# Optimization experiments

Hardware: AMD Instinct MI355X
Metric: run time of the kernel (lower is better)

The kernel has to match this reference:

```python
import math
import jax, jax.numpy as jnp
import numpy as np

H, C, PQ, PV = 8, 256, 8, 12   # no_heads, c_hidden, no_qk_points, no_v_points
INF, EPS = 1e5, 1e-8

def quat_to_rot(q):
    w, x, y, z = q[..., 0], q[..., 1], q[..., 2], q[..., 3]
    r = jnp.stack([
        1 - 2*(y*y + z*z), 2*(x*y - w*z),     2*(x*z + w*y),
        2*(x*y + w*z),     1 - 2*(x*x + z*z), 2*(y*z - w*x),
        2*(x*z - w*y),     2*(y*z + w*x),     1 - 2*(x*x + y*y),
    ], axis=-1)
    return r.reshape(q.shape[:-1] + (3, 3))

def setup_inputs() -> dict:
    key = jax.random.key(0)
    ks = jax.random.split(key, 16)
    B, N, CS, CZ = 1, 512, 384, 128
    s = jax.random.normal(ks[0], (B, N, CS), jnp.float32)
    z = jax.random.normal(ks[1], (B, N, N, CZ), jnp.float32) * 0.1
    quat = jax.random.normal(ks[2], (B, N, 4), jnp.float32)
    quat = quat / jnp.linalg.norm(quat, axis=-1, keepdims=True)
    rot = quat_to_rot(quat)                       # [B,N,3,3] valid rotations
    trans = jax.random.normal(ks[3], (B, N, 3), jnp.float32) * 10.0
    mask = jnp.ones((B, N), jnp.float32)
    g = lambda k, sh: jax.random.normal(k, sh, jnp.float32) * 0.02
    params = dict(
        wq=g(ks[4], (CS, H*C)), bq=jnp.zeros((H*C,), jnp.float32),
        wkv=g(ks[5], (CS, 2*H*C)), bkv=jnp.zeros((2*H*C,), jnp.float32),
        wqp=g(ks[6], (CS, H*PQ*3)), bqp=jnp.zeros((H*PQ*3,), jnp.float32),
        wkvp=g(ks[7], (CS, H*(PQ+PV)*3)), bkvp=jnp.zeros((H*(PQ+PV)*3,), jnp.float32),
        wb=g(ks[8], (CZ, H)), bb=jnp.zeros((H,), jnp.float32),
        wz=g(ks[9], (CZ, CZ//4)), bz=jnp.zeros((CZ//4,), jnp.float32),
        head_weights=jnp.full((H,), 0.541324854612918, jnp.float32),  # softplus^-1(1)
        wo=g(ks[10], (H*(C + 4*PV + CZ//4), CS)), bo=jnp.zeros((CS,), jnp.float32),
    )
    return dict(s=s, z=z, rot=rot, trans=trans, mask=mask, **params)

def reference(s, z, rot, trans, mask, wq, bq, wkv, bkv, wqp, bqp, wkvp, bkvp, wb, bb, wz, bz, head_weights, wo, bo):
    B, N, CS = s.shape
    q = (s @ wq + bq).reshape(B, N, H, C)
    kv = (s @ wkv + bkv).reshape(B, N, H, 2 * C)
    k, v = kv[..., :C], kv[..., C:]

    def split_pts(x):  # torch split-into-3 + stack(-1): [B,N,3*M] -> [B,N,M,3]
        return jnp.moveaxis(x.reshape(B, N, 3, -1), -2, -1)

    def apply_rigid(p):  # global frame: R @ p + t
        return jnp.einsum('bnij,bnpj->bnpi', rot, p) + trans[:, :, None, :]

    q_pts = apply_rigid(split_pts(s @ wqp + bqp)).reshape(B, N, H, PQ, 3)
    kv_pts = apply_rigid(split_pts(s @ wkvp + bkvp)).reshape(B, N, H, PQ + PV, 3)
    k_pts, v_pts = kv_pts[..., :PQ, :], kv_pts[..., PQ:, :]

    b_bias = z @ wb + bb                                  # [B,Ni,Nj,H]
    a = jnp.einsum('bihc,bjhc->bhij', q, k) * math.sqrt(1.0 / (3 * C))
    a = a + math.sqrt(1.0 / 3) * jnp.moveaxis(b_bias, -1, 1)

    disp = q_pts[:, :, None] - k_pts[:, None]             # [B,Ni,Nj,H,PQ,3]
    pt_att = jnp.sum(disp * disp, axis=-1)                # [B,Ni,Nj,H,PQ]
    hw = jax.nn.softplus(head_weights) * math.sqrt(1.0 / (3 * (PQ * 9.0 / 2)))
    pt_att = -0.5 * jnp.sum(pt_att * hw[None, None, None, :, None], axis=-1)  # [B,Ni,Nj,H]

    sq_mask = INF * (mask[:, :, None] * mask[:, None, :] - 1.0)
    a = a + jnp.moveaxis(pt_att, -1, 1) + sq_mask[:, None]
    a = jax.nn.softmax(a, axis=-1)                        # [B,H,Ni,Nj]

    o = jnp.einsum('bhij,bjhc->bihc', a, v).reshape(B, N, H * C)

    o_pt = jnp.einsum('bhij,bjhpd->bihpd', a, v_pts)      # [B,N,H,PV,3] global
    o_pt = jnp.einsum('bnji,bnhpj->bnhpi', rot, o_pt - trans[:, :, None, None, :])  # invert_apply
    o_pt_norm = jnp.sqrt(jnp.sum(o_pt * o_pt, axis=-1) + EPS).reshape(B, N, H * PV)
    o_pt_flat = o_pt.reshape(B, N, H * PV, 3)

    pair_z = z @ wz + bz                                  # [B,Ni,Nj,CZ//4]
    o_pair = jnp.einsum('bhij,bijd->bihd', a, pair_z).reshape(B, N, -1)

    feats = jnp.concatenate(
        [o, o_pt_flat[..., 0], o_pt_flat[..., 1], o_pt_flat[..., 2], o_pt_norm, o_pair], axis=-1)
    return feats @ wo + bo
```

## Files before the change

kernel.cpp:

```cpp
#include <hip/hip_runtime.h>


#define OFF_QBH    0
#define OFF_KBH    524288
#define OFF_VB     1048576
#define OFF_QPRAW  2097152
#define OFF_KVPRAW 2195456
#define OFF_QPTS   2441216
#define OFF_KVPTS  2539520
#define OFF_BBIAS  2785280
#define OFF_PAIRZT 3833856
#define OFF_ATTNH  8028160
#define OFF_FEATSB 9076736
#define OFF_WCAT   9764864
#define OFF_WTALL  9767936
#define OFF_VPT    11082752
#define OFF_WOT    11803648
#define OFF_QPTH   12319744
#define OFF_QPTL   12385280
#define OFF_KPTH   12450816
#define OFF_KPTL   12516352
#define OFF_QP2    12581888
#define OFF_KP2    12585984

typedef __attribute__((ext_vector_type(8))) short short8;
typedef __attribute__((ext_vector_type(4))) float f32x4;

__device__ __forceinline__ unsigned short f2bf(float f) {
  union { float f; unsigned u; } v; v.f = f;
  unsigned u = v.u;
  unsigned r = (u + 0x7fffu + ((u >> 16) & 1u)) >> 16;
  return (unsigned short)r;
}
__device__ __forceinline__ float bf2f(unsigned short h) {
  union { unsigned u; float f; } v; v.u = ((unsigned)h) << 16; return v.f;
}
__device__ __forceinline__ short8 pack8(float4 a, float4 b) {
  short8 r;
  r[0] = (short)f2bf(a.x); r[1] = (short)f2bf(a.y);
  r[2] = (short)f2bf(a.z); r[3] = (short)f2bf(a.w);
  r[4] = (short)f2bf(b.x); r[5] = (short)f2bf(b.y);
  r[6] = (short)f2bf(b.z); r[7] = (short)f2bf(b.w);
  return r;
}

__global__ __launch_bounds__(256) void prep_wT_all(
    const float* __restrict__ wq, const float* __restrict__ wkv,
    const float* __restrict__ wqp, const float* __restrict__ wkvp,
    unsigned short* __restrict__ wTall) {
  const int ntile = blockIdx.x, kt = blockIdx.y;
  const float* src; int Nsrc, nloc0;
  const int ng0 = ntile * 64;
  if (ntile < 32)      { src = wq;   Nsrc = 2048; nloc0 = ng0; }
  else if (ntile < 96) { src = wkv;  Nsrc = 4096; nloc0 = ng0 - 2048; }
  else if (ntile < 99) { src = wqp;  Nsrc = 192;  nloc0 = ng0 - 6144; }
  else                 { src = wkvp; Nsrc = 480;  nloc0 = ng0 - 6336; }
  __shared__ float tile[64][65];
  const int t = threadIdx.x;
  const int r = t >> 2, cs = (t & 3) * 16;
#pragma unroll
  for (int i = 0; i < 16; i += 4) {
    int n = nloc0 + cs + i;
    float4 v;
    if (n + 3 < Nsrc) v = *(const float4*)(src + (size_t)(kt * 64 + r) * Nsrc + n);
    else {
      v.x = (n + 0 < Nsrc) ? src[(size_t)(kt * 64 + r) * Nsrc + n + 0] : 0.f;
      v.y = (n + 1 < Nsrc) ? src[(size_t)(kt * 64 + r) * Nsrc + n + 1] : 0.f;
      v.z = (n + 2 < Nsrc) ? src[(size_t)(kt * 64 + r) * Nsrc + n + 2] : 0.f;
      v.w = (n + 3 < Nsrc) ? src[(size_t)(kt * 64 + r) * Nsrc + n + 3] : 0.f;
    }
    tile[r][cs + i + 0] = v.x; tile[r][cs + i + 1] = v.y;
    tile[r][cs + i + 2] = v.z; tile[r][cs + i + 3] = v.w;
  }
  __syncthreads();
  const int nr = t >> 2, ks = (t & 3) * 16;
  unsigned short ov[16];
#pragma unroll
  for (int i = 0; i < 16; i++) ov[i] = f2bf(tile[ks + i][nr]);
  unsigned short* dst = wTall + (size_t)(ng0 + nr) * 384 + kt * 64 + ks;
  *(uint4*)(dst) = *(const uint4*)&ov[0];
  *(uint4*)(dst + 8) = *(const uint4*)&ov[8];
}

__global__ __launch_bounds__(256) void prep_woT(
    const float* __restrict__ wo, unsigned short* __restrict__ woT) {
  const int kt = blockIdx.x, ntile = blockIdx.y;
  __shared__ float tile[64][65];
  const int t = threadIdx.x;
  const int r = t >> 2, cs = (t & 3) * 16;
#pragma unroll
  for (int i = 0; i < 16; i += 4) {
    float4 v = *(const float4*)(wo + (size_t)(kt * 64 + r) * 384 + ntile * 64 + cs + i);
    tile[r][cs + i + 0] = v.x; tile[r][cs + i + 1] = v.y;
    tile[r][cs + i + 2] = v.z; tile[r][cs + i + 3] = v.w;
  }
  __syncthreads();
  const int nr = t >> 2, ks = (t & 3) * 16;
  unsigned short ov[16];
#pragma unroll
  for (int i = 0; i < 16; i++) ov[i] = f2bf(tile[ks + i][nr]);
  unsigned short* dst = woT + (size_t)(ntile * 64 + nr) * 2688 + kt * 64 + ks;
  *(uint4*)(dst) = *(const uint4*)&ov[0];
  *(uint4*)(dst + 8) = *(const uint4*)&ov[8];
}

__global__ __launch_bounds__(256) void proj_mfma(
    const float* __restrict__ s, const unsigned short* __restrict__ wTall,
    const float* __restrict__ bq, const float* __restrict__ bkv,
    const float* __restrict__ bqp, const float* __restrict__ bkvp,
    unsigned short* __restrict__ qbh, unsigned short* __restrict__ kbh,
    float* __restrict__ vb, float* __restrict__ qpraw, float* __restrict__ kvpraw) {
  const int bx = blockIdx.x, row0 = blockIdx.y * 64;
  const int lane = threadIdx.x & 63, wv = threadIdx.x >> 6;
  const int quad = lane >> 4, m = lane & 15;
  const int n0 = bx * 64;
  const float* srow = s + (size_t)(row0 + wv * 16 + m) * 384;
  f32x4 acc[4];
#pragma unroll
  for (int nt = 0; nt < 4; nt++) acc[nt] = (f32x4){0.f, 0.f, 0.f, 0.f};

#pragma unroll
  for (int ksx = 0; ksx < 12; ksx++) {
    const int c0 = ksx * 32 + quad * 8;
    float4 a0 = *(const float4*)(srow + c0);
    float4 a1 = *(const float4*)(srow + c0 + 4);
    short8 af = pack8(a0, a1);
#pragma unroll
    for (int nt = 0; nt < 4; nt++) {
      short8 bf = *(const short8*)(wTall + (size_t)(n0 + nt * 16 + m) * 384 + c0);
      acc[nt] = __builtin_amdgcn_mfma_f32_16x16x32_bf16(af, bf, acc[nt], 0, 0, 0);
    }
  }

  const int rbase = row0 + wv * 16 + quad * 4;
#pragma unroll
  for (int nt = 0; nt < 4; nt++) {
    const int col = n0 + nt * 16 + m;
    if (n0 < 2048) {
      const float bias = bq[col];
#pragma unroll
      for (int r = 0; r < 4; r++)
        qbh[(size_t)(rbase + r) * 2048 + col] = f2bf(acc[nt][r] + bias);
    } else if (n0 < 6144) {
      const int ckv = col - 2048;
      const float bias = bkv[ckv];
      const int hh = ckv >> 9, c = ckv & 511;
      if (c < 256) {
#pragma unroll
        for (int r = 0; r < 4; r++)
          kbh[(size_t)(rbase + r) * 2048 + hh * 256 + c] = f2bf(acc[nt][r] + bias);
      } else {
#pragma unroll
        for (int r = 0; r < 4; r++)
          vb[(size_t)(rbase + r) * 2048 + hh * 256 + (c - 256)] = acc[nt][r] + bias;
      }
    } else if (n0 < 6336) {
      const int cq = col - 6144;
      const float bias = bqp[cq];
#pragma unroll
      for (int r = 0; r < 4; r++)
        qpraw[(size_t)(rbase + r) * 192 + cq] = acc[nt][r] + bias;
    } else {
      const int ck = col - 6336;
      if (ck < 480) {
        const float bias = bkvp[ck];
#pragma unroll
        for (int r = 0; r < 4; r++)
          kvpraw[(size_t)(rbase + r) * 480 + ck] = acc[nt][r] + bias;
      }
    }
  }
}

__global__ __launch_bounds__(256) void rigid_pts(
    const float* __restrict__ qpraw, const float* __restrict__ kvpraw,
    const float* __restrict__ rot, const float* __restrict__ trans,
    float* __restrict__ qpts, float* __restrict__ kvpts) {
  int gid = blockIdx.x * 256 + threadIdx.x;
  int n = gid / 224, r = gid % 224;
  const float* R  = rot + n * 9;
  const float* tr = trans + n * 3;
  float px, py, pz; float* dst;
  if (r < 64) {
    const float* src = qpraw + (size_t)n * 192;
    px = src[r]; py = src[64 + r]; pz = src[128 + r];
    dst = qpts + ((size_t)n * 64 + r) * 3;
  } else {
    int p = r - 64;
    const float* src = kvpraw + (size_t)n * 480;
    px = src[p]; py = src[160 + p]; pz = src[320 + p];
    dst = kvpts + ((size_t)n * 160 + p) * 3;
  }
  dst[0] = R[0] * px + R[1] * py + R[2] * pz + tr[0];
  dst[1] = R[3] * px + R[4] * py + R[5] * pz + tr[1];
  dst[2] = R[6] * px + R[7] * py + R[8] * pz + tr[2];
}

__global__ __launch_bounds__(256) void pts_planes(
    const float* __restrict__ qpts, const float* __restrict__ kvpts,
    unsigned short* __restrict__ qptH, unsigned short* __restrict__ qptL,
    unsigned short* __restrict__ kptH, unsigned short* __restrict__ kptL,
    float* __restrict__ qp2g, float* __restrict__ kp2g) {
  const int row = blockIdx.x * 256 + threadIdx.x;
  const int h = blockIdx.y;
  {
    const float* src = qpts + ((size_t)row * 64 + h * 8) * 3;
    unsigned short hi[32], lo[32]; float s2 = 0.f;
#pragma unroll
    for (int w = 0; w < 24; w++) {
      float x = src[w];
      hi[w] = f2bf(x); lo[w] = f2bf(x - bf2f(hi[w]));
      s2 += x * x;
    }
#pragma unroll
    for (int w = 24; w < 32; w++) { hi[w] = 0; lo[w] = 0; }
    unsigned short* dh = qptH + ((size_t)h * 512 + row) * 32;
    unsigned short* dl = qptL + ((size_t)h * 512 + row) * 32;
#pragma unroll
    for (int g = 0; g < 4; g++) {
      *(uint4*)(dh + g * 8) = *(const uint4*)&hi[g * 8];
      *(uint4*)(dl + g * 8) = *(const uint4*)&lo[g * 8];
    }
    qp2g[h * 512 + row] = s2;
  }
  {
    const float* src = kvpts + ((size_t)row * 160 + h * 20) * 3;
    unsigned short hi[32], lo[32]; float s2 = 0.f;
#pragma unroll
    for (int w = 0; w < 24; w++) {
      float x = src[w];
      hi[w] = f2bf(x); lo[w] = f2bf(x - bf2f(hi[w]));
      s2 += x * x;
    }
#pragma unroll
    for (int w = 24; w < 32; w++) { hi[w] = 0; lo[w] = 0; }
    unsigned short* dh = kptH + ((size_t)h * 512 + row) * 32;
    unsigned short* dl = kptL + ((size_t)h * 512 + row) * 32;
#pragma unroll
    for (int g = 0; g < 4; g++) {
      *(uint4*)(dh + g * 8) = *(const uint4*)&hi[g * 8];
      *(uint4*)(dl + g * 8) = *(const uint4*)&lo[g * 8];
    }
    kp2g[h * 512 + row] = s2;
  }
}

__global__ __launch_bounds__(256) void prep_wT(
    const float* __restrict__ wb, const float* __restrict__ wz,
    unsigned short* __restrict__ wT) {
  int l = blockIdx.x * 256 + threadIdx.x;
  if (l < 6144) {
    int n = l >> 7, k = l & 127;
    float v = (n < 8) ? wb[k * 8 + n] * 0.5773502691896258f
                      : (n < 40 ? wz[k * 32 + (n - 8)] : 0.f);
    wT[l] = f2bf(v);
  }
}

__global__ __launch_bounds__(256) void zpass_mfma(
    const float* __restrict__ z, const unsigned short* __restrict__ wT,
    const float* __restrict__ bb, const float* __restrict__ bz,
    unsigned short* __restrict__ bbias_tb, unsigned short* __restrict__ pairzT) {
  __shared__ __align__(16) unsigned short lb[4][8][16];
  __shared__ __align__(16) unsigned short lp[4][32][16];
  const int lane = threadIdx.x & 63;
  const int wave = threadIdx.x >> 6;
  const int quad = lane >> 4, m = lane & 15;
  const int tile = blockIdx.x * 4 + wave;
  const int row0 = tile * 16;

  short8 bf[3][4];
#pragma unroll
  for (int nt = 0; nt < 3; nt++)
#pragma unroll
    for (int s = 0; s < 4; s++)
      bf[nt][s] = *(const short8*)(wT + (size_t)(nt * 16 + m) * 128 + s * 32 + quad * 8);

  float bias[3];
#pragma unroll
  for (int nt = 0; nt < 3; nt++) {
    int c = nt * 16 + m;
    bias[nt] = (c < 8) ? 0.5773502691896258f * bb[c] : (c < 40 ? bz[c - 8] : 0.f);
  }

  f32x4 acc[3];
#pragma unroll
  for (int nt = 0; nt < 3; nt++) acc[nt] = (f32x4){0.f, 0.f, 0.f, 0.f};

  const float* zr = z + (size_t)(row0 + m) * 128 + quad * 8;
#pragma unroll
  for (int s = 0; s < 4; s++) {
    float4 a0 = *(const float4*)(zr + s * 32);
    float4 a1 = *(const float4*)(zr + s * 32 + 4);
    short8 af = pack8(a0, a1);
#pragma unroll
    for (int nt = 0; nt < 3; nt++)
      acc[nt] = __builtin_amdgcn_mfma_f32_16x16x32_bf16(af, bf[nt][s], acc[nt], 0, 0, 0);
  }

#pragma unroll
  for (int nt = 0; nt < 3; nt++) {
    const int c = nt * 16 + m;
#pragma unroll
    for (int r = 0; r < 4; r++) {
      const float v = acc[nt][r] + bias[nt];
      const int jl = quad * 4 + r;
      if (c < 8)       lb[wave][c][jl] = f2bf(v);
      else if (c < 40) lp[wave][c - 8][jl] = f2bf(v);
    }
  }
  const int i = row0 >> 9, j0 = row0 & 511;
  if (lane < 16) {
    int c = lane >> 1, half = lane & 1;
    uint4 val = *(const uint4*)&lb[wave][c][half * 8];
    *(uint4*)(bbias_tb + (size_t)c * 262144 + row0 + half * 8) = val;
  }
  {
    int d = lane >> 1, half = lane & 1;
    uint4 val = *(const uint4*)&lp[wave][d][half * 8];
    *(uint4*)(pairzT + ((size_t)i * 32 + d) * 512 + j0 + half * 8) = val;
  }
}

__global__ __launch_bounds__(256) void vpt_prep(
    const float* __restrict__ vb, const float* __restrict__ kvpts,
    unsigned short* __restrict__ vptT) {
  const int jt = blockIdx.x, h = blockIdx.y, part = blockIdx.z;
  const int j0 = jt * 64, t = threadIdx.x;
  if (part < 4) {
    __shared__ float tile[64][65];
    const int c0 = part * 64;
    const int r = t >> 2, cs = (t & 3) * 16;
#pragma unroll
    for (int ii = 0; ii < 16; ii += 4) {
      float4 v = *(const float4*)(vb + (size_t)(j0 + r) * 2048 + h * 256 + c0 + cs + ii);
      tile[r][cs + ii + 0] = v.x; tile[r][cs + ii + 1] = v.y;
      tile[r][cs + ii + 2] = v.z; tile[r][cs + ii + 3] = v.w;
    }
    __syncthreads();
    const int cl = t >> 2, js = (t & 3) * 16;
    unsigned short ov[16];
#pragma unroll
    for (int x = 0; x < 16; x++) ov[x] = f2bf(tile[js + x][cl]);
    unsigned short* dst = vptT + ((size_t)h * 352 + c0 + cl) * 512 + j0 + js;
    *(uint4*)dst = *(const uint4*)&ov[0];
    *(uint4*)(dst + 8) = *(const uint4*)&ov[8];
  } else {
    __shared__ float lds[64][37];
    for (int l = t; l < 64 * 36; l += 256) {
      int jl = l / 36, w = l % 36;
      lds[jl][w] = kvpts[((size_t)(j0 + jl) * 160 + h * 20 + 8) * 3 + w];
    }
    __syncthreads();
#pragma unroll
    for (int step = 0; step < 3; step++) {
      int chunk = t + 256 * step;
      int row = chunk >> 3, js = (chunk & 7) * 8;
      unsigned short ov[8];
#pragma unroll
      for (int x = 0; x < 8; x++) {
        int w = (row < 48) ? row : row - 48;
        float f = (w < 36) ? lds[js + x][w] : 0.f;
        unsigned short hi = f2bf(f);
        ov[x] = (row < 48) ? hi : f2bf(f - bf2f(hi));
      }
      *(uint4*)(vptT + ((size_t)h * 352 + 256 + row) * 512 + j0 + js) = *(const uint4*)&ov[0];
    }
  }
}

__global__ __launch_bounds__(256) void logits_fused(
    const unsigned short* __restrict__ qbh, const unsigned short* __restrict__ kbh,
    const unsigned short* __restrict__ qptH, const unsigned short* __restrict__ qptL,
    const unsigned short* __restrict__ kptH, const unsigned short* __restrict__ kptL,
    const float* __restrict__ qp2g, const float* __restrict__ kp2g,
    const unsigned short* __restrict__ bbias_tb, const float* __restrict__ mask,
    const float* __restrict__ hwp, const unsigned short* __restrict__ vptT,
    const float* __restrict__ rot, const float* __restrict__ trans,
    unsigned short* __restrict__ attnh, unsigned short* __restrict__ featsb) {
  const int it = blockIdx.x, h = blockIdx.y;
  const int i0 = it * 16;
  __shared__ __align__(16) unsigned short sth[4][16][136], stl[4][16][136];
  __shared__ float redm[16][4], reds[16][4];
  __shared__ float lds_h[16][48], lds_l[16][48];
  const int t = threadIdx.x;
  const int lane = t & 63, wv = t >> 6;
  const int quad = lane >> 4, m = lane & 15;
  const int jw0 = wv * 128;

  f32x4 acc[8];
#pragma unroll
  for (int nt = 0; nt < 8; nt++) acc[nt] = (f32x4){0.f, 0.f, 0.f, 0.f};
  const unsigned short* qrow = qbh + (size_t)(i0 + m) * 2048 + h * 256;
#pragma unroll
  for (int s = 0; s < 8; s++) {
    short8 af = *(const short8*)(qrow + s * 32 + quad * 8);
#pragma unroll
    for (int nt = 0; nt < 8; nt++) {
      short8 bfr = *(const short8*)(kbh + (size_t)(jw0 + nt * 16 + m) * 2048 + h * 256 + s * 32 + quad * 8);
      acc[nt] = __builtin_amdgcn_mfma_f32_16x16x32_bf16(af, bfr, acc[nt], 0, 0, 0);
    }
  }

  short8 aqh = *(const short8*)(qptH + ((size_t)h * 512 + i0 + m) * 32 + quad * 8);
  short8 aql = *(const short8*)(qptL + ((size_t)h * 512 + i0 + m) * 32 + quad * 8);
  f32x4 accp[8];
#pragma unroll
  for (int nt = 0; nt < 8; nt++) {
    const size_t krow = ((size_t)h * 512 + jw0 + nt * 16 + m) * 32 + quad * 8;
    short8 bkh = *(const short8*)(kptH + krow);
    short8 bkl = *(const short8*)(kptL + krow);
    f32x4 p = (f32x4){0.f, 0.f, 0.f, 0.f};
    p = __builtin_amdgcn_mfma_f32_16x16x32_bf16(aqh, bkh, p, 0, 0, 0);
    p = __builtin_amdgcn_mfma_f32_16x16x32_bf16(aqh, bkl, p, 0, 0, 0);
    p = __builtin_amdgcn_mfma_f32_16x16x32_bf16(aql, bkh, p, 0, 0, 0);
    accp[nt] = p;
  }

  const float c1 = 0.03608439182435161f;
  const float hw = log1pf(expf(hwp[h])) * 0.09622504486493764f;
  float qp2v[4];
#pragma unroll
  for (int r = 0; r < 4; r++) qp2v[r] = qp2g[h * 512 + i0 + quad * 4 + r];
  float lg[8][4];
  float rmax[4] = {-1e30f, -1e30f, -1e30f, -1e30f};
#pragma unroll
  for (int nt = 0; nt < 8; nt++) {
    const int j = jw0 + nt * 16 + m;
    const float kp2v = kp2g[h * 512 + j];
    const float mj = mask[j];
#pragma unroll
    for (int r = 0; r < 4; r++) {
      const int il = quad * 4 + r;
      const float pt = qp2v[r] + kp2v - 2.f * accp[nt][r];
      float v = c1 * acc[nt][r]
              + bf2f(bbias_tb[(size_t)h * 262144 + (size_t)(i0 + il) * 512 + j])
              - 0.5f * hw * pt
              + 100000.f * (mask[i0 + il] * mj - 1.f);
      lg[nt][r] = v;
      rmax[r] = fmaxf(rmax[r], v);
    }
  }
#pragma unroll
  for (int r = 0; r < 4; r++) {
#pragma unroll
    for (int off = 1; off < 16; off <<= 1) rmax[r] = fmaxf(rmax[r], __shfl_xor(rmax[r], off));
  }
  if (m == 0) {
#pragma unroll
    for (int r = 0; r < 4; r++) redm[quad * 4 + r][wv] = rmax[r];
  }
  __syncthreads();
  float rowm[4], rsum[4];
#pragma unroll
  for (int r = 0; r < 4; r++) {
    const int il = quad * 4 + r;
    rowm[r] = fmaxf(fmaxf(redm[il][0], redm[il][1]), fmaxf(redm[il][2], redm[il][3]));
    rsum[r] = 0.f;
  }
#pragma unroll
  for (int nt = 0; nt < 8; nt++)
#pragma unroll
    for (int r = 0; r < 4; r++) {
      float e = __expf(lg[nt][r] - rowm[r]);
      lg[nt][r] = e;
      rsum[r] += e;
    }
#pragma unroll
  for (int r = 0; r < 4; r++) {
#pragma unroll
    for (int off = 1; off < 16; off <<= 1) rsum[r] += __shfl_xor(rsum[r], off);
  }
  if (m == 0) {
#pragma unroll
    for (int r = 0; r < 4; r++) reds[quad * 4 + r][wv] = rsum[r];
  }
  __syncthreads();
  float inv[4];
#pragma unroll
  for (int r = 0; r < 4; r++) {
    const int il = quad * 4 + r;
    inv[r] = 1.f / (reds[il][0] + reds[il][1] + reds[il][2] + reds[il][3]);
  }
#pragma unroll
  for (int nt = 0; nt < 8; nt++)
#pragma unroll
    for (int r = 0; r < 4; r++) {
      const int il = quad * 4 + r;
      float a = lg[nt][r] * inv[r];
      unsigned short hi = f2bf(a);
      sth[wv][il][nt * 16 + m] = hi;
      stl[wv][il][nt * 16 + m] = f2bf(a - bf2f(hi));
    }
  __syncthreads();
#pragma unroll
  for (int step = 0; step < 4; step++) {
    const int idx = lane + 64 * step;
    const int il = idx >> 4, seg = idx & 15;
    uint4 vh = *(const uint4*)&sth[wv][il][seg * 8];
    *(uint4*)(attnh + ((size_t)h * 512 + i0 + il) * 512 + jw0 + seg * 8) = vh;
  }

  const int nt0 = wv * 6;
  const int ncnt = (wv == 3) ? 4 : 6;
  f32x4 vacc[6];
#pragma unroll
  for (int k = 0; k < 6; k++) vacc[k] = (f32x4){0.f, 0.f, 0.f, 0.f};
  const unsigned short* vbase = vptT + (size_t)h * 352 * 512;
#pragma unroll
  for (int s = 0; s < 16; s++) {
    const int wsrc = s >> 2, col = (s & 3) * 32 + quad * 8;
    short8 ah = *(const short8*)&sth[wsrc][m][col];
    short8 al = *(const short8*)&stl[wsrc][m][col];
    const int ko = s * 32 + quad * 8;
#pragma unroll
    for (int k = 0; k < 6; k++) {
      if (k < ncnt) {
        const int nt = nt0 + k;
        short8 bfr = *(const short8*)(vbase + (size_t)(nt * 16 + m) * 512 + ko);
        vacc[k] = __builtin_amdgcn_mfma_f32_16x16x32_bf16(ah, bfr, vacc[k], 0, 0, 0);
        if (nt >= 16 && nt < 19)
          vacc[k] = __builtin_amdgcn_mfma_f32_16x16x32_bf16(al, bfr, vacc[k], 0, 0, 0);
      }
    }
  }
#pragma unroll
  for (int k = 0; k < 6; k++) {
    if (k < ncnt) {
      const int nt = nt0 + k;
      if (nt < 16) {
#pragma unroll
        for (int r = 0; r < 4; r++)
          featsb[(size_t)(i0 + quad * 4 + r) * 2688 + h * 256 + nt * 16 + m] = f2bf(vacc[k][r]);
      } else if (nt < 19) {
        const int w = (nt - 16) * 16 + m;
#pragma unroll
        for (int r = 0; r < 4; r++) if (w < 36) lds_h[quad * 4 + r][w] = vacc[k][r];
      } else {
        const int w = (nt - 19) * 16 + m;
#pragma unroll
        for (int r = 0; r < 4; r++) if (w < 36) lds_l[quad * 4 + r][w] = vacc[k][r];
      }
    }
  }
  __syncthreads();
  if (t < 192) {
    const int il = t / 12, p = t % 12, irow = i0 + il;
    const float* R = rot + irow * 9;
    const float* tr = trans + irow * 3;
    float x  = lds_h[il][p * 3 + 0] + lds_l[il][p * 3 + 0] - tr[0];
    float y  = lds_h[il][p * 3 + 1] + lds_l[il][p * 3 + 1] - tr[1];
    float zz = lds_h[il][p * 3 + 2] + lds_l[il][p * 3 + 2] - tr[2];
    float o0 = R[0] * x + R[3] * y + R[6] * zz;
    float o1 = R[1] * x + R[4] * y + R[7] * zz;
    float o2 = R[2] * x + R[5] * y + R[8] * zz;
    float nrm = sqrtf(o0 * o0 + o1 * o1 + o2 * o2 + 1e-8f);
    unsigned short* fr = featsb + (size_t)irow * 2688 + 2048;
    fr[h * 12 + p]       = f2bf(o0);
    fr[96 + h * 12 + p]  = f2bf(o1);
    fr[192 + h * 12 + p] = f2bf(o2);
    fr[288 + h * 12 + p] = f2bf(nrm);
  }
}

__global__ __launch_bounds__(256) void o_pair_mfma(
    const unsigned short* __restrict__ attnh, const unsigned short* __restrict__ pairzT,
    unsigned short* __restrict__ featsb) {
  const int lane = threadIdx.x & 63, wv = threadIdx.x >> 6;
  const int quad = lane >> 4, m = lane & 15;
  const int i = blockIdx.x * 4 + wv;
  f32x4 acc[2];
  acc[0] = (f32x4){0.f, 0.f, 0.f, 0.f};
  acc[1] = (f32x4){0.f, 0.f, 0.f, 0.f};
#pragma unroll
  for (int s = 0; s < 16; s++) {
    const int ko = s * 32 + quad * 8;
    short8 af = *(const short8*)(attnh + (size_t)(m & 7) * 262144 + (size_t)i * 512 + ko);
#pragma unroll
    for (int nt = 0; nt < 2; nt++) {
      short8 bfr = *(const short8*)(pairzT + ((size_t)i * 32 + nt * 16 + m) * 512 + ko);
      acc[nt] = __builtin_amdgcn_mfma_f32_16x16x32_bf16(af, bfr, acc[nt], 0, 0, 0);
    }
  }
  if (quad < 2) {
#pragma unroll
    for (int nt = 0; nt < 2; nt++)
#pragma unroll
      for (int r = 0; r < 4; r++) {
        const int hh = quad * 4 + r, d = nt * 16 + m;
        featsb[(size_t)i * 2688 + 2432 + hh * 32 + d] = f2bf(acc[nt][r]);
      }
  }
}

__global__ __launch_bounds__(256) void out_mfma(
    const unsigned short* __restrict__ featsb, const unsigned short* __restrict__ woT,
    const float* __restrict__ bo, float* __restrict__ out) {
  const int it = blockIdx.x, ng = blockIdx.y;
  const int lane = threadIdx.x & 63, wv = threadIdx.x >> 6;
  const int quad = lane >> 4, m = lane & 15;
  const int i0 = it * 16, n0 = (ng * 4 + wv) * 16;
  const unsigned short* arow = featsb + (size_t)(i0 + m) * 2688;
  const unsigned short* brow = woT + (size_t)(n0 + m) * 2688;
  f32x4 acc = (f32x4){0.f, 0.f, 0.f, 0.f};
#pragma unroll 4
  for (int s = 0; s < 84; s++) {
    const int ko = s * 32 + quad * 8;
    short8 af = *(const short8*)(arow + ko);
    short8 bf = *(const short8*)(brow + ko);
    acc = __builtin_amdgcn_mfma_f32_16x16x32_bf16(af, bf, acc, 0, 0, 0);
  }
  const float bias = bo[n0 + m];
#pragma unroll
  for (int r = 0; r < 4; r++)
    out[(size_t)(i0 + quad * 4 + r) * 384 + n0 + m] = acc[r] + bias;
}

extern "C" void kernel_launch(void* const* d_in, const int* in_sizes, int n_in,
                              void* d_out, int out_size, void* d_ws, size_t ws_size,
                              hipStream_t stream) {
  const float* s     = (const float*)d_in[0];
  const float* z     = (const float*)d_in[1];
  const float* rot   = (const float*)d_in[2];
  const float* trans = (const float*)d_in[3];
  const float* mask  = (const float*)d_in[4];
  const float* wq    = (const float*)d_in[5];
  const float* bq    = (const float*)d_in[6];
  const float* wkv   = (const float*)d_in[7];
  const float* bkv   = (const float*)d_in[8];
  const float* wqp   = (const float*)d_in[9];
  const float* bqp   = (const float*)d_in[10];
  const float* wkvp  = (const float*)d_in[11];
  const float* bkvp  = (const float*)d_in[12];
  const float* wb    = (const float*)d_in[13];
  const float* bb    = (const float*)d_in[14];
  const float* wz    = (const float*)d_in[15];
  const float* bz    = (const float*)d_in[16];
  const float* hwp   = (const float*)d_in[17];
  const float* wo    = (const float*)d_in[18];
  const float* bo    = (const float*)d_in[19];
  float* out = (float*)d_out;

  float* ws = (float*)d_ws;
  unsigned short* qbh   = (unsigned short*)(ws + OFF_QBH);
  unsigned short* kbh   = (unsigned short*)(ws + OFF_KBH);
  float* vb      = ws + OFF_VB;
  float* qpraw   = ws + OFF_QPRAW;
  float* kvpraw  = ws + OFF_KVPRAW;
  float* qpts    = ws + OFF_QPTS;
  float* kvpts   = ws + OFF_KVPTS;
  unsigned short* bbias_tb = (unsigned short*)(ws + OFF_BBIAS);
  unsigned short* pairzT   = (unsigned short*)(ws + OFF_PAIRZT);
  unsigned short* attnh    = (unsigned short*)(ws + OFF_ATTNH);
  unsigned short* featsb   = (unsigned short*)(ws + OFF_FEATSB);
  unsigned short* wT    = (unsigned short*)(ws + OFF_WCAT);
  unsigned short* wTall = (unsigned short*)(ws + OFF_WTALL);
  unsigned short* vptT  = (unsigned short*)(ws + OFF_VPT);
  unsigned short* woT   = (unsigned short*)(ws + OFF_WOT);
  unsigned short* qptH  = (unsigned short*)(ws + OFF_QPTH);
  unsigned short* qptL  = (unsigned short*)(ws + OFF_QPTL);
  unsigned short* kptH  = (unsigned short*)(ws + OFF_KPTH);
  unsigned short* kptL  = (unsigned short*)(ws + OFF_KPTL);
  float* qp2g = ws + OFF_QP2;
  float* kp2g = ws + OFF_KP2;

  prep_wT_all<<<dim3(107, 6), 256, 0, stream>>>(wq, wkv, wqp, wkvp, wTall);
  prep_wT<<<24, 256, 0, stream>>>(wb, wz, wT);
  prep_woT<<<dim3(42, 6), 256, 0, stream>>>(wo, woT);
  proj_mfma<<<dim3(107, 8), 256, 0, stream>>>(s, wTall, bq, bkv, bqp, bkvp,
                                              qbh, kbh, vb, qpraw, kvpraw);
  rigid_pts<<<448, 256, 0, stream>>>(qpraw, kvpraw, rot, trans, qpts, kvpts);
  pts_planes<<<dim3(2, 8), 256, 0, stream>>>(qpts, kvpts, qptH, qptL, kptH, kptL, qp2g, kp2g);
  zpass_mfma<<<4096, 256, 0, stream>>>(z, wT, bb, bz, bbias_tb, pairzT);
  vpt_prep<<<dim3(8, 8, 5), 256, 0, stream>>>(vb, kvpts, vptT);
  logits_fused<<<dim3(32, 8), 256, 0, stream>>>(qbh, kbh, qptH, qptL, kptH, kptL,
                                                qp2g, kp2g, bbias_tb, mask, hwp,
                                                vptT, rot, trans, attnh, featsb);
  o_pair_mfma<<<128, 256, 0, stream>>>(attnh, pairzT, featsb);
  out_mfma<<<dim3(32, 6), 256, 0, stream>>>(featsb, woT, bo, out);
}
```

Before: 372.0 us.

## Merge prep kernels, pre-convert s to bf16, and widen logits_fused to 8 waves

Three weight-prep kernels are merged into a single launch, which also converts s to bf16 once. proj_mfma then loads bf16 s directly instead of packing it from fp32 in every block. logits_fused moves from 256 to 512 threads, so each wave covers 64 key columns instead of 128 and the value/point output tiles are spread over 8 waves. This cuts launch count and redundant conversion work and raises parallelism in the attention kernel, at the cost of more shared-memory reduction traffic and more synchronisation across waves.

```diff
diff --git a/kernel.cpp b/kernel.cpp
--- a/kernel.cpp
+++ b/kernel.cpp
@@ -22,6 +22,7 @@
 #define OFF_KPTL   12516352
 #define OFF_QP2    12581888
 #define OFF_KP2    12585984
+#define OFF_SBF    12590080
 
 typedef __attribute__((ext_vector_type(8))) short short8;
 typedef __attribute__((ext_vector_type(4))) float f32x4;
@@ -44,68 +45,83 @@
   return r;
 }
 
-__global__ __launch_bounds__(256) void prep_wT_all(
+__global__ __launch_bounds__(256) void prep_all(
     const float* __restrict__ wq, const float* __restrict__ wkv,
     const float* __restrict__ wqp, const float* __restrict__ wkvp,
-    unsigned short* __restrict__ wTall) {
-  const int ntile = blockIdx.x, kt = blockIdx.y;
-  const float* src; int Nsrc, nloc0;
-  const int ng0 = ntile * 64;
-  if (ntile < 32)      { src = wq;   Nsrc = 2048; nloc0 = ng0; }
-  else if (ntile < 96) { src = wkv;  Nsrc = 4096; nloc0 = ng0 - 2048; }
-  else if (ntile < 99) { src = wqp;  Nsrc = 192;  nloc0 = ng0 - 6144; }
-  else                 { src = wkvp; Nsrc = 480;  nloc0 = ng0 - 6336; }
+    const float* __restrict__ wo, const float* __restrict__ wb,
+    const float* __restrict__ wz, const float* __restrict__ s,
+    unsigned short* __restrict__ wTall, unsigned short* __restrict__ woT,
+    unsigned short* __restrict__ wT, unsigned short* __restrict__ sbf) {
   __shared__ float tile[64][65];
-  const int t = threadIdx.x;
-  const int r = t >> 2, cs = (t & 3) * 16;
-#pragma unroll
-  for (int i = 0; i < 16; i += 4) {
-    int n = nloc0 + cs + i;
-    float4 v;
-    if (n + 3 < Nsrc) v = *(const float4*)(src + (size_t)(kt * 64 + r) * Nsrc + n);
-    else {
-      v.x = (n + 0 < Nsrc) ? src[(size_t)(kt * 64 + r) * Nsrc + n + 0] : 0.f;
-      v.y = (n + 1 < Nsrc) ? src[(size_t)(kt * 64 + r) * Nsrc + n + 1] : 0.f;
-      v.z = (n + 2 < Nsrc) ? src[(size_t)(kt * 64 + r) * Nsrc + n + 2] : 0.f;
-      v.w = (n + 3 < Nsrc) ? src[(size_t)(kt * 64 + r) * Nsrc + n + 3] : 0.f;
-    }
-    tile[r][cs + i + 0] = v.x; tile[r][cs + i + 1] = v.y;
-    tile[r][cs + i + 2] = v.z; tile[r][cs + i + 3] = v.w;
-  }
-  __syncthreads();
-  const int nr = t >> 2, ks = (t & 3) * 16;
-  unsigned short ov[16];
-#pragma unroll
-  for (int i = 0; i < 16; i++) ov[i] = f2bf(tile[ks + i][nr]);
-  unsigned short* dst = wTall + (size_t)(ng0 + nr) * 384 + kt * 64 + ks;
-  *(uint4*)(dst) = *(const uint4*)&ov[0];
-  *(uint4*)(dst + 8) = *(const uint4*)&ov[8];
-}
-
-__global__ __launch_bounds__(256) void prep_woT(
-    const float* __restrict__ wo, unsigned short* __restrict__ woT) {
-  const int kt = blockIdx.x, ntile = blockIdx.y;
-  __shared__ float tile[64][65];
-  const int t = threadIdx.x;
-  const int r = t >> 2, cs = (t & 3) * 16;
-#pragma unroll
-  for (int i = 0; i < 16; i += 4) {
-    float4 v = *(const float4*)(wo + (size_t)(kt * 64 + r) * 384 + ntile * 64 + cs + i);
-    tile[r][cs + i + 0] = v.x; tile[r][cs + i + 1] = v.y;
-    tile[r][cs + i + 2] = v.z; tile[r][cs + i + 3] = v.w;
-  }
-  __syncthreads();
-  const int nr = t >> 2, ks = (t & 3) * 16;
-  unsigned short ov[16];
-#pragma unroll
-  for (int i = 0; i < 16; i++) ov[i] = f2bf(tile[ks + i][nr]);
-  unsigned short* dst = woT + (size_t)(ntile * 64 + nr) * 2688 + kt * 64 + ks;
-  *(uint4*)(dst) = *(const uint4*)&ov[0];
-  *(uint4*)(dst + 8) = *(const uint4*)&ov[8];
+  const int b = blockIdx.x, t = threadIdx.x;
+  if (b < 642) {
+    const int ntile = b % 107, kt = b / 107;
+    const float* src; int Nsrc, nloc0;
+    const int ng0 = ntile * 64;
+    if (ntile < 32)      { src = wq;   Nsrc = 2048; nloc0 = ng0; }
+    else if (ntile < 96) { src = wkv;  Nsrc = 4096; nloc0 = ng0 - 2048; }
+    else if (ntile < 99) { src = wqp;  Nsrc = 192;  nloc0 = ng0 - 6144; }
+    else                 { src = wkvp; Nsrc = 480;  nloc0 = ng0 - 6336; }
+    const int r = t >> 2, cs = (t & 3) * 16;
+#pragma unroll
+    for (int i = 0; i < 16; i += 4) {
+      int n = nloc0 + cs + i;
+      float4 v;
+      if (n + 3 < Nsrc) v = *(const float4*)(src + (size_t)(kt * 64 + r) * Nsrc + n);
+      else {
+        v.x = (n + 0 < Nsrc) ? src[(size_t)(kt * 64 + r) * Nsrc + n + 0] : 0.f;
+        v.y = (n + 1 < Nsrc) ? src[(size_t)(kt * 64 + r) * Nsrc + n + 1] : 0.f;
+        v.z = (n + 2 < Nsrc) ? src[(size_t)(kt * 64 + r) * Nsrc + n + 2] : 0.f;
+        v.w = (n + 3 < Nsrc) ? src[(size_t)(kt * 64 + r) * Nsrc + n + 3] : 0.f;
+      }
+      tile[r][cs + i + 0] = v.x; tile[r][cs + i + 1] = v.y;
+      tile[r][cs + i + 2] = v.z; tile[r][cs + i + 3] = v.w;
+    }
+    __syncthreads();
+    const int nr = t >> 2, ks = (t & 3) * 16;
+    unsigned short ov[16];
+#pragma unroll
+    for (int i = 0; i < 16; i++) ov[i] = f2bf(tile[ks + i][nr]);
+    unsigned short* dst = wTall + (size_t)(ng0 + nr) * 384 + kt * 64 + ks;
+    *(uint4*)(dst) = *(const uint4*)&ov[0];
+    *(uint4*)(dst + 8) = *(const uint4*)&ov[8];
+  } else if (b < 894) {
+    const int idx = b - 642;
+    const int kt = idx % 42, ntile = idx / 42;
+    const int r = t >> 2, cs = (t & 3) * 16;
+#pragma unroll
+    for (int i = 0; i < 16; i += 4) {
+      float4 v = *(const float4*)(wo + (size_t)(kt * 64 + r) * 384 + ntile * 64 + cs + i);
+      tile[r][cs + i + 0] = v.x; tile[r][cs + i + 1] = v.y;
+      tile[r][cs + i + 2] = v.z; tile[r][cs + i + 3] = v.w;
+    }
+    __syncthreads();
+    const int nr = t >> 2, ks = (t & 3) * 16;
+    unsigned short ov[16];
+#pragma unroll
+    for (int i = 0; i < 16; i++) ov[i] = f2bf(tile[ks + i][nr]);
+    unsigned short* dst = woT + (size_t)(ntile * 64 + nr) * 2688 + kt * 64 + ks;
+    *(uint4*)(dst) = *(const uint4*)&ov[0];
+    *(uint4*)(dst + 8) = *(const uint4*)&ov[8];
+  } else if (b < 918) {
+    const int l = (b - 894) * 256 + t;
+    if (l < 6144) {
+      int n = l >> 7, k = l & 127;
+      float v = (n < 8) ? wb[k * 8 + n] * 0.5773502691896258f
+                        : (n < 40 ? wz[k * 32 + (n - 8)] : 0.f);
+      wT[l] = f2bf(v);
+    }
+  } else {
+    const int gid = (b - 918) * 256 + t;
+    const int off = gid * 8;
+    float4 a0 = *(const float4*)(s + off);
+    float4 a1 = *(const float4*)(s + off + 4);
+    *(short8*)(sbf + off) = pack8(a0, a1);
+  }
 }
 
 __global__ __launch_bounds__(256) void proj_mfma(
-    const float* __restrict__ s, const unsigned short* __restrict__ wTall,
+    const unsigned short* __restrict__ sbf, const unsigned short* __restrict__ wTall,
     const float* __restrict__ bq, const float* __restrict__ bkv,
     const float* __restrict__ bqp, const float* __restrict__ bkvp,
     unsigned short* __restrict__ qbh, unsigned short* __restrict__ kbh,
@@ -114,7 +130,7 @@
   const int lane = threadIdx.x & 63, wv = threadIdx.x >> 6;
   const int quad = lane >> 4, m = lane & 15;
   const int n0 = bx * 64;
-  const float* srow = s + (size_t)(row0 + wv * 16 + m) * 384;
+  const unsigned short* srow = sbf + (size_t)(row0 + wv * 16 + m) * 384;
   f32x4 acc[4];
 #pragma unroll
   for (int nt = 0; nt < 4; nt++) acc[nt] = (f32x4){0.f, 0.f, 0.f, 0.f};
@@ -122,9 +138,7 @@
 #pragma unroll
   for (int ksx = 0; ksx < 12; ksx++) {
     const int c0 = ksx * 32 + quad * 8;
-    float4 a0 = *(const float4*)(srow + c0);
-    float4 a1 = *(const float4*)(srow + c0 + 4);
-    short8 af = pack8(a0, a1);
+    short8 af = *(const short8*)(srow + c0);
 #pragma unroll
     for (int nt = 0; nt < 4; nt++) {
       short8 bf = *(const short8*)(wTall + (size_t)(n0 + nt * 16 + m) * 384 + c0);
@@ -245,18 +259,6 @@
   }
 }
 
-__global__ __launch_bounds__(256) void prep_wT(
-    const float* __restrict__ wb, const float* __restrict__ wz,
-    unsigned short* __restrict__ wT) {
-  int l = blockIdx.x * 256 + threadIdx.x;
-  if (l < 6144) {
-    int n = l >> 7, k = l & 127;
-    float v = (n < 8) ? wb[k * 8 + n] * 0.5773502691896258f
-                      : (n < 40 ? wz[k * 32 + (n - 8)] : 0.f);
-    wT[l] = f2bf(v);
-  }
-}
-
 __global__ __launch_bounds__(256) void zpass_mfma(
     const float* __restrict__ z, const unsigned short* __restrict__ wT,
     const float* __restrict__ bb, const float* __restrict__ bz,
@@ -369,7 +371,7 @@
   }
 }
 
-__global__ __launch_bounds__(256) void logits_fused(
+__global__ __launch_bounds__(512) void logits_fused(
     const unsigned short* __restrict__ qbh, const unsigned short* __restrict__ kbh,
     const unsigned short* __restrict__ qptH, const unsigned short* __restrict__ qptL,
     const unsigned short* __restrict__ kptH, const unsigned short* __restrict__ kptL,
@@ -380,23 +382,23 @@
     unsigned short* __restrict__ attnh, unsigned short* __restrict__ featsb) {
   const int it = blockIdx.x, h = blockIdx.y;
   const int i0 = it * 16;
-  __shared__ __align__(16) unsigned short sth[4][16][136], stl[4][16][136];
-  __shared__ float redm[16][4], reds[16][4];
+  __shared__ __align__(16) unsigned short sth[8][16][72], stl[8][16][72];
+  __shared__ float redm[16][8], reds[16][8];
   __shared__ float lds_h[16][48], lds_l[16][48];
   const int t = threadIdx.x;
   const int lane = t & 63, wv = t >> 6;
   const int quad = lane >> 4, m = lane & 15;
-  const int jw0 = wv * 128;
-
-  f32x4 acc[8];
-#pragma unroll
-  for (int nt = 0; nt < 8; nt++) acc[nt] = (f32x4){0.f, 0.f, 0.f, 0.f};
+  const int jw0 = wv * 64;
+
+  f32x4 acc[4];
+#pragma unroll
+  for (int nt = 0; nt < 4; nt++) acc[nt] = (f32x4){0.f, 0.f, 0.f, 0.f};
   const unsigned short* qrow = qbh + (size_t)(i0 + m) * 2048 + h * 256;
 #pragma unroll
   for (int s = 0; s < 8; s++) {
     short8 af = *(const short8*)(qrow + s * 32 + quad * 8);
 #pragma unroll
-    for (int nt = 0; nt < 8; nt++) {
+    for (int nt = 0; nt < 4; nt++) {
       short8 bfr = *(const short8*)(kbh + (size_t)(jw0 + nt * 16 + m) * 2048 + h * 256 + s * 32 + quad * 8);
       acc[nt] = __builtin_amdgcn_mfma_f32_16x16x32_bf16(af, bfr, acc[nt], 0, 0, 0);
     }
@@ -404,9 +406,9 @@
 
   short8 aqh = *(const short8*)(qptH + ((size_t)h * 512 + i0 + m) * 32 + quad * 8);
   short8 aql = *(const short8*)(qptL + ((size_t)h * 512 + i0 + m) * 32 + quad * 8);
-  f32x4 accp[8];
-#pragma unroll
-  for (int nt = 0; nt < 8; nt++) {
+  f32x4 accp[4];
+#pragma unroll
+  for (int nt = 0; nt < 4; nt++) {
     const size_t krow = ((size_t)h * 512 + jw0 + nt * 16 + m) * 32 + quad * 8;
     short8 bkh = *(const short8*)(kptH + krow);
     short8 bkl = *(const short8*)(kptL + krow);
@@ -422,10 +424,10 @@
   float qp2v[4];
 #pragma unroll
   for (int r = 0; r < 4; r++) qp2v[r] = qp2g[h * 512 + i0 + quad * 4 + r];
-  float lg[8][4];
+  float lg[4][4];
   float rmax[4] = {-1e30f, -1e30f, -1e30f, -1e30f};
 #pragma unroll
-  for (int nt = 0; nt < 8; nt++) {
+  for (int nt = 0; nt < 4; nt++) {
     const int j = jw0 + nt * 16 + m;
     const float kp2v = kp2g[h * 512 + j];
     const float mj = mask[j];
@@ -455,11 +457,13 @@
 #pragma unroll
   for (int r = 0; r < 4; r++) {
     const int il = quad * 4 + r;
-    rowm[r] = fmaxf(fmaxf(redm[il][0], redm[il][1]), fmaxf(redm[il][2], redm[il][3]));
+    float m0 = fmaxf(fmaxf(redm[il][0], redm[il][1]), fmaxf(redm[il][2], redm[il][3]));
+    float m1 = fmaxf(fmaxf(redm[il][4], redm[il][5]), fmaxf(redm[il][6], redm[il][7]));
+    rowm[r] = fmaxf(m0, m1);
     rsum[r] = 0.f;
   }
 #pragma unroll
-  for (int nt = 0; nt < 8; nt++)
+  for (int nt = 0; nt < 4; nt++)
 #pragma unroll
     for (int r = 0; r < 4; r++) {
       float e = __expf(lg[nt][r] - rowm[r]);
@@ -480,10 +484,12 @@
 #pragma unroll
   for (int r = 0; r < 4; r++) {
     const int il = quad * 4 + r;
-    inv[r] = 1.f / (reds[il][0] + reds[il][1] + reds[il][2] + reds[il][3]);
-  }
-#pragma unroll
-  for (int nt = 0; nt < 8; nt++)
+    float s0 = (reds[il][0] + reds[il][1]) + (reds[il][2] + reds[il][3]);
+    float s1 = (reds[il][4] + reds[il][5]) + (reds[il][6] + reds[il][7]);
+    inv[r] = 1.f / (s0 + s1);
+  }
+#pragma unroll
+  for (int nt = 0; nt < 4; nt++)
 #pragma unroll
     for (int r = 0; r < 4; r++) {
       const int il = quad * 4 + r;
@@ -494,27 +500,27 @@
     }
   __syncthreads();
 #pragma unroll
-  for (int step = 0; step < 4; step++) {
+  for (int step = 0; step < 2; step++) {
     const int idx = lane + 64 * step;
-    const int il = idx >> 4, seg = idx & 15;
+    const int il = idx >> 3, seg = idx & 7;
     uint4 vh = *(const uint4*)&sth[wv][il][seg * 8];
     *(uint4*)(attnh + ((size_t)h * 512 + i0 + il) * 512 + jw0 + seg * 8) = vh;
   }
 
-  const int nt0 = wv * 6;
-  const int ncnt = (wv == 3) ? 4 : 6;
-  f32x4 vacc[6];
-#pragma unroll
-  for (int k = 0; k < 6; k++) vacc[k] = (f32x4){0.f, 0.f, 0.f, 0.f};
+  const int nt0 = (wv < 6) ? wv * 3 : 18 + (wv - 6) * 2;
+  const int ncnt = (wv < 6) ? 3 : 2;
+  f32x4 vacc[3];
+#pragma unroll
+  for (int k = 0; k < 3; k++) vacc[k] = (f32x4){0.f, 0.f, 0.f, 0.f};
   const unsigned short* vbase = vptT + (size_t)h * 352 * 512;
 #pragma unroll
   for (int s = 0; s < 16; s++) {
-    const int wsrc = s >> 2, col = (s & 3) * 32 + quad * 8;
+    const int wsrc = s >> 1, col = (s & 1) * 32 + quad * 8;
     short8 ah = *(const short8*)&sth[wsrc][m][col];
     short8 al = *(const short8*)&stl[wsrc][m][col];
     const int ko = s * 32 + quad * 8;
 #pragma unroll
-    for (int k = 0; k < 6; k++) {
+    for (int k = 0; k < 3; k++) {
       if (k < ncnt) {
         const int nt = nt0 + k;
         short8 bfr = *(const short8*)(vbase + (size_t)(nt * 16 + m) * 512 + ko);
@@ -525,7 +531,7 @@
     }
   }
 #pragma unroll
-  for (int k = 0; k < 6; k++) {
+  for (int k = 0; k < 3; k++) {
     if (k < ncnt) {
       const int nt = nt0 + k;
       if (nt < 16) {
@@ -663,17 +669,17 @@
   unsigned short* kptL  = (unsigned short*)(ws + OFF_KPTL);
   float* qp2g = ws + OFF_QP2;
   float* kp2g = ws + OFF_KP2;
-
-  prep_wT_all<<<dim3(107, 6), 256, 0, stream>>>(wq, wkv, wqp, wkvp, wTall);
-  prep_wT<<<24, 256, 0, stream>>>(wb, wz, wT);
-  prep_woT<<<dim3(42, 6), 256, 0, stream>>>(wo, woT);
-  proj_mfma<<<dim3(107, 8), 256, 0, stream>>>(s, wTall, bq, bkv, bqp, bkvp,
+  unsigned short* sbf = (unsigned short*)(ws + OFF_SBF);
+
+  prep_all<<<1014, 256, 0, stream>>>(wq, wkv, wqp, wkvp, wo, wb, wz, s,
+                                     wTall, woT, wT, sbf);
+  proj_mfma<<<dim3(107, 8), 256, 0, stream>>>(sbf, wTall, bq, bkv, bqp, bkvp,
                                               qbh, kbh, vb, qpraw, kvpraw);
   rigid_pts<<<448, 256, 0, stream>>>(qpraw, kvpraw, rot, trans, qpts, kvpts);
   pts_planes<<<dim3(2, 8), 256, 0, stream>>>(qpts, kvpts, qptH, qptL, kptH, kptL, qp2g, kp2g);
   zpass_mfma<<<4096, 256, 0, stream>>>(z, wT, bb, bz, bbias_tb, pairzT);
   vpt_prep<<<dim3(8, 8, 5), 256, 0, stream>>>(vb, kvpts, vptT);
-  logits_fused<<<dim3(32, 8), 256, 0, stream>>>(qbh, kbh, qptH, qptL, kptH, kptL,
+  logits_fused<<<dim3(32, 8), 512, 0, stream>>>(qbh, kbh, qptH, qptL, kptH, kptL,
                                                 qp2g, kp2g, bbias_tb, mask, hwp,
                                                 vptT, rot, trans, attnh, featsb);
   o_pair_mfma<<<128, 256, 0, stream>>>(attnh, pairzT, featsb);
```

Measured after the change: 352.0 us. 1.06x faster.
